# Kernel tuning notes

Hardware: AMD Instinct MI355X
Metric: run time of the kernel (lower is better)

Reference implementation:

```python
import jax, jax.numpy as jnp
import numpy as np

B, N, E = 4, 10000, 160000
D, H, HID, DE = 128, 4, 128, 16
DK = HID // H


def setup_inputs() -> dict:
    key = jax.random.key(0)
    ks = jax.random.split(key, 16)
    w = lambda k, shape: jax.random.normal(k, shape, jnp.float32) * 0.02
    return {
        "x": jax.random.normal(ks[0], (B, N, D), jnp.float32),
        "edge_index": jax.random.randint(ks[1], (2, E), 0, N, dtype=jnp.int32),
        "edge_attr": jax.random.normal(ks[2], (E, DE), jnp.float32),
        "Wq": w(ks[3], (D, HID)), "bq": jnp.zeros((HID,), jnp.float32),
        "Wk": w(ks[4], (D, HID)), "bk": jnp.zeros((HID,), jnp.float32),
        "Wv": w(ks[5], (D, HID)), "bv": jnp.zeros((HID,), jnp.float32),
        "Wf": w(ks[6], (DE, 2 * HID)), "bf": jnp.zeros((2 * HID,), jnp.float32),
        "Wo": w(ks[7], (HID, D)), "bo": jnp.zeros((D,), jnp.float32),
        "ln_g": jnp.ones((D,), jnp.float32), "ln_b": jnp.zeros((D,), jnp.float32),
    }


def reference(x, edge_index, edge_attr, Wq, bq, Wk, bk, Wv, bv, Wf, bf, Wo, bo, ln_g, ln_b):
    src, dst = edge_index[0], edge_index[1]
    # node projections -> [B, N, H, DK]
    Q = (x @ Wq + bq).reshape(B, N, H, DK)
    K = (x @ Wk + bk).reshape(B, N, H, DK)
    V = (x @ Wv + bv).reshape(B, N, H, DK)
    # edge gathers -> [B, E, H, DK]
    q_e, k_e, v_e = Q[:, dst], K[:, src], V[:, src]
    # FiLM modulation of keys (edge-conditioned, shared across batch)
    gamma, beta = jnp.split(edge_attr @ Wf + bf, 2, axis=-1)
    gamma = gamma.reshape(1, E, H, DK)
    beta = beta.reshape(1, E, H, DK)
    k_e = k_e * (1.0 + gamma) + beta
    logits = (q_e * k_e).sum(-1) / np.sqrt(DK).astype(np.float32)  # [B, E, H]

    def seg_softmax(lg):  # lg: [E, H], softmax over edges sharing a dst node
        m = jax.ops.segment_max(lg, dst, num_segments=N)       # [N, H]
        ex = jnp.exp(lg - m[dst])
        s = jax.ops.segment_sum(ex, dst, num_segments=N)        # [N, H]
        return ex / s[dst]

    att = jax.vmap(seg_softmax)(logits)                         # [B, E, H]
    msg = att[..., None] * v_e                                  # [B, E, H, DK]
    agg = jax.vmap(lambda m: jax.ops.segment_sum(m, dst, num_segments=N))(msg)
    y = agg.reshape(B, N, HID) @ Wo + bo                        # [B, N, D]
    h = x + y  # dropout is identity in eval mode
    mu = h.mean(-1, keepdims=True)
    var = ((h - mu) ** 2).mean(-1, keepdims=True)
    return (h - mu) / jnp.sqrt(var + 1e-5) * ln_g + ln_b
```

## Files before the change

kernel.cpp:

```cpp
#include <hip/hip_runtime.h>
#include <hip/hip_bf16.h>

#define B_ 4
#define N_ 10000
#define E_ 160000
#define D_ 128
#define H_ 4
#define HID_ 128
#define DK_ 32
#define DE_ 16
#define PGRID 2048
#define QKV_BLKS 625
#define FILM_BLKS 1024
#define HIST_BLKS 625

typedef __attribute__((ext_vector_type(8))) short short8v;
typedef __attribute__((ext_vector_type(4))) short short4v;
typedef __attribute__((ext_vector_type(4))) float f32x4;
typedef __attribute__((ext_vector_type(2))) float f32x2;

__device__ __forceinline__ short bfb(float f) {
  union { float f; unsigned u; } c; c.f = f;
  unsigned u = c.u + 0x7FFFu + ((c.u >> 16) & 1u);
  return (short)(u >> 16);
}
__device__ __forceinline__ float b2f(unsigned short u) {
  union { unsigned u; float f; } c; c.u = ((unsigned)u) << 16;
  return c.f;
}
__device__ __forceinline__ f32x2 fp8lo(unsigned u) {
  return __builtin_amdgcn_cvt_pk_f32_fp8((int)u, false);
}
__device__ __forceinline__ f32x2 fp8hi(unsigned u) {
  return __builtin_amdgcn_cvt_pk_f32_fp8((int)u, true);
}
__device__ __forceinline__ int pk4fp8(float a, float b, float c, float d) {
  int r = __builtin_amdgcn_cvt_pk_fp8_f32(a, b, 0, false);
  r = __builtin_amdgcn_cvt_pk_fp8_f32(c, d, r, true);
  return r;
}

__global__ __launch_bounds__(256) void wt_prep(
    const float* __restrict__ Wq, const float* __restrict__ Wk,
    const float* __restrict__ Wv, const float* __restrict__ Wo,
    const float* __restrict__ Wf,
    short* __restrict__ wt, short* __restrict__ wfb) {
  const int blk = blockIdx.x;
  if (blk < 256) {
    const float* Ws[4] = {Wq, Wk, Wv, Wo};
    const int i = blk * 256 + threadIdx.x;
    const int m = i >> 14;
    const int k = (i >> 7) & 127;
    const int n = i & 127;
    wt[(size_t)m * 16384 + n * 128 + k] = bfb(Ws[m][k * 128 + n]);
  } else {
    const int i = (blk - 256) * 256 + threadIdx.x;
    const int col = i >> 5;
    const int k = i & 31;
    wfb[col * 32 + k] = (k < DE_) ? bfb(Wf[k * 256 + col]) : (short)0;
  }
}

__global__ __launch_bounds__(256) void phase1(
    const float* __restrict__ x, const short* __restrict__ wt,
    const float* __restrict__ bq, const float* __restrict__ bk,
    const float* __restrict__ bv,
    unsigned short* __restrict__ Qb, unsigned char* __restrict__ kv8,
    const float* __restrict__ ea, const short* __restrict__ wfb,
    const float* __restrict__ bf, unsigned char* __restrict__ film8,
    const int* __restrict__ ei, int* __restrict__ cnt) {
  const int blk = blockIdx.x;

  if (blk < QKV_BLKS) {
    __shared__ short xs[4][16][136];
    const int wave = threadIdx.x >> 6;
    const int lane = threadIdx.x & 63;
    const int ln15 = lane & 15;
    const int g    = lane >> 4;
    const long rowBase = ((long)blk * 4 + wave) * 16;

    for (int i = lane; i < 16 * 32; i += 64) {
      const int r  = i >> 5;
      const int c4 = (i & 31) * 4;
      const float4 v = *(const float4*)(x + (rowBase + r) * 128 + c4);
      short4v sv; sv.x = bfb(v.x); sv.y = bfb(v.y); sv.z = bfb(v.z); sv.w = bfb(v.w);
      *(short4v*)&xs[wave][r][c4] = sv;
    }
    __syncthreads();

    short8v af[4];
#pragma unroll
    for (int kk = 0; kk < 4; ++kk)
      af[kk] = *(const short8v*)&xs[wave][ln15][kk * 32 + g * 8];

    const float* bs[3] = {bq, bk, bv};

    int bbv4[4], nnv[4];
#pragma unroll
    for (int r = 0; r < 4; ++r) {
      const long row = rowBase + g * 4 + r;
      bbv4[r] = (int)(row / N_);
      nnv[r] = (int)(row - (long)bbv4[r] * N_);
    }

#pragma unroll
    for (int m = 0; m < 3; ++m) {
      const short* Wt = wt + (size_t)m * 16384;
      f32x4 acc[8];
#pragma unroll
      for (int cb = 0; cb < 8; ++cb) acc[cb] = (f32x4){0.f, 0.f, 0.f, 0.f};

#pragma unroll
      for (int kk = 0; kk < 4; ++kk) {
#pragma unroll
        for (int cb = 0; cb < 8; ++cb) {
          const short8v bfr =
              *(const short8v*)(Wt + (ln15 * 8 + cb) * 128 + kk * 32 + g * 8);
          acc[cb] = __builtin_amdgcn_mfma_f32_16x16x32_bf16(af[kk], bfr, acc[cb], 0, 0, 0);
        }
      }

      const float* bias = bs[m];
      float bvv[8];
#pragma unroll
      for (int cb = 0; cb < 8; ++cb) bvv[cb] = bias[ln15 * 8 + cb];

#pragma unroll
      for (int r = 0; r < 4; ++r) {
        if (m == 0) {
          const long row = rowBase + g * 4 + r;
          short8v qs;
#pragma unroll
          for (int cb = 0; cb < 8; ++cb) qs[cb] = bfb(acc[cb][r] + bvv[cb]);
          *(short8v*)(Qb + row * 128 + ln15 * 8) = qs;
        } else {
          const int d0 = pk4fp8(acc[0][r] + bvv[0], acc[1][r] + bvv[1],
                                acc[2][r] + bvv[2], acc[3][r] + bvv[3]);
          const int d1 = pk4fp8(acc[4][r] + bvv[4], acc[5][r] + bvv[5],
                                acc[6][r] + bvv[6], acc[7][r] + bvv[7]);
          uint2 st; st.x = (unsigned)d0; st.y = (unsigned)d1;
          *(uint2*)(kv8 + (((size_t)nnv[r] * 4 + bbv4[r]) << 8) + (m - 1) * 128 +
                    ln15 * 8) = st;
        }
      }
    }
  } else if (blk < QKV_BLKS + FILM_BLKS) {
    const int fb_  = blk - QKV_BLKS;
    const int wave = threadIdx.x >> 6;
    const int lane = threadIdx.x & 63;
    const int ln15 = lane & 15;
    const int g    = lane >> 4;

    short8v wf[16];
#pragma unroll
    for (int cb = 0; cb < 16; ++cb)
      wf[cb] = *(const short8v*)(wfb + (ln15 * 16 + cb) * 32 + g * 8);
    float fbias[16];
#pragma unroll
    for (int cb = 0; cb < 16; ++cb) fbias[cb] = bf[ln15 * 16 + cb];

    for (int tile = fb_ * 4 + wave; tile < E_ / 16; tile += FILM_BLKS * 4) {
      const int e0 = tile * 16;
      short8v af = {0, 0, 0, 0, 0, 0, 0, 0};
      if (g < 2) {
        const float* ap = ea + (size_t)(e0 + ln15) * 16 + g * 8;
        const float4 a0 = *(const float4*)ap;
        const float4 a1 = *(const float4*)(ap + 4);
        af[0] = bfb(a0.x); af[1] = bfb(a0.y); af[2] = bfb(a0.z); af[3] = bfb(a0.w);
        af[4] = bfb(a1.x); af[5] = bfb(a1.y); af[6] = bfb(a1.z); af[7] = bfb(a1.w);
      }

#pragma unroll
      for (int half = 0; half < 2; ++half) {
        f32x4 acc[8];
#pragma unroll
        for (int c8 = 0; c8 < 8; ++c8) {
          acc[c8] = (f32x4){0.f, 0.f, 0.f, 0.f};
          acc[c8] = __builtin_amdgcn_mfma_f32_16x16x32_bf16(af, wf[half * 8 + c8],
                                                            acc[c8], 0, 0, 0);
        }
#pragma unroll
        for (int r = 0; r < 4; ++r) {
          const int d0 = pk4fp8(acc[0][r] + fbias[half * 8 + 0],
                                acc[1][r] + fbias[half * 8 + 1],
                                acc[2][r] + fbias[half * 8 + 2],
                                acc[3][r] + fbias[half * 8 + 3]);
          const int d1 = pk4fp8(acc[4][r] + fbias[half * 8 + 4],
                                acc[5][r] + fbias[half * 8 + 5],
                                acc[6][r] + fbias[half * 8 + 6],
                                acc[7][r] + fbias[half * 8 + 7]);
          uint2 st; st.x = (unsigned)d0; st.y = (unsigned)d1;
          *(uint2*)(film8 + (size_t)(e0 + 4 * g + r) * 256 + ln15 * 16 + half * 8) = st;
        }
      }
    }
  } else {
    const int e = (blk - QKV_BLKS - FILM_BLKS) * 256 + threadIdx.x;
    if (e < E_) atomicAdd(&cnt[ei[E_ + e]], 1);
  }
}

__global__ __launch_bounds__(1024) void csr_scan(const int* __restrict__ cnt,
                                                 int* __restrict__ rowptr,
                                                 int* __restrict__ fill) {
  __shared__ int part[1024];
  const int t = threadIdx.x;
  int local[10];
  int sum = 0;
#pragma unroll
  for (int i = 0; i < 10; ++i) {
    const int idx = t * 10 + i;
    local[i] = sum;
    sum += (idx < N_) ? cnt[idx] : 0;
  }
  part[t] = sum;
  __syncthreads();
  for (int off = 1; off < 1024; off <<= 1) {
    const int v = (t >= off) ? part[t - off] : 0;
    __syncthreads();
    part[t] += v;
    __syncthreads();
  }
  const int excl = (t == 0) ? 0 : part[t - 1];
#pragma unroll
  for (int i = 0; i < 10; ++i) {
    const int idx = t * 10 + i;
    if (idx <= N_) {
      const int o = excl + local[i];
      rowptr[idx] = o;
      if (idx < N_) fill[idx] = o;
    }
  }
}

__global__ __launch_bounds__(256) void csr_scatter(
    const int* __restrict__ ei, int* __restrict__ fill,
    int* __restrict__ esrc, int* __restrict__ eord) {
  const int e = blockIdx.x * 256 + threadIdx.x;
  if (e < E_) {
    const int dst = ei[E_ + e];
    const int pos = atomicAdd(&fill[dst], 1);
    esrc[pos] = ei[e];
    eord[pos] = e;
  }
}

__global__ __launch_bounds__(256) void fused_attn(
    const int* __restrict__ rowptr, const int* __restrict__ esrc,
    const int* __restrict__ eord, const unsigned char* __restrict__ film8,
    const unsigned short* __restrict__ Qb,
    const unsigned char* __restrict__ kv8, float* __restrict__ agg) {
  const int wave = threadIdx.x >> 6;
  const int lane = threadIdx.x & 63;
  const int e2 = lane >> 5;
  const int dh = (lane >> 4) & 1;
  const int b  = (lane >> 2) & 3;
  const int h  = lane & 3;
  const int col0 = h * 32 + dh * 16;

  for (int node = blockIdx.x * 4 + wave; node < N_; node += PGRID * 4) {
    const int beg = rowptr[node], end = rowptr[node + 1];

    float q[16];
    {
      const unsigned short* qp = Qb + ((size_t)b * N_ + node) * 128 + col0;
      const short8v t0 = *(const short8v*)qp;
      const short8v t1 = *(const short8v*)(qp + 8);
#pragma unroll
      for (int j = 0; j < 8; ++j) {
        q[j]     = b2f((unsigned short)t0[j]);
        q[8 + j] = b2f((unsigned short)t1[j]);
      }
    }
    float acc[16];
#pragma unroll
    for (int d = 0; d < 16; ++d) acc[d] = 0.f;
    float se = 0.f;

    for (int i0 = beg; i0 < end; i0 += 2) {
      const int ii = i0 + e2;
      const bool valid = ii < end;
      const int ic = valid ? ii : i0;
      const int src = esrc[ic];
      const int de  = eord[ic];
      const unsigned char* kp = kv8 + ((((size_t)src << 2) + b) << 8) + col0;
      const unsigned char* fp = film8 + (size_t)de * 256 + col0;
      const uint4 kw = *(const uint4*)kp;
      const uint4 vw = *(const uint4*)(kp + 128);
      const uint4 gw = *(const uint4*)fp;
      const uint4 tw = *(const uint4*)(fp + 128);
      const unsigned ks[4] = {kw.x, kw.y, kw.z, kw.w};
      const unsigned vs[4] = {vw.x, vw.y, vw.z, vw.w};
      const unsigned gs[4] = {gw.x, gw.y, gw.z, gw.w};
      const unsigned ts[4] = {tw.x, tw.y, tw.z, tw.w};

      float pacc[4] = {0.f, 0.f, 0.f, 0.f};
#pragma unroll
      for (int w = 0; w < 4; ++w) {
        const f32x2 k0 = fp8lo(ks[w]), k1 = fp8hi(ks[w]);
        const f32x2 g0 = fp8lo(gs[w]), g1 = fp8hi(gs[w]);
        const f32x2 t0 = fp8lo(ts[w]), t1 = fp8hi(ts[w]);
        float km;
        km = k0.x + fmaf(k0.x, g0.x, t0.x); pacc[w] = fmaf(q[4*w+0], km, pacc[w]);
        km = k0.y + fmaf(k0.y, g0.y, t0.y); pacc[w] = fmaf(q[4*w+1], km, pacc[w]);
        km = k1.x + fmaf(k1.x, g1.x, t1.x); pacc[w] = fmaf(q[4*w+2], km, pacc[w]);
        km = k1.y + fmaf(k1.y, g1.y, t1.y); pacc[w] = fmaf(q[4*w+3], km, pacc[w]);
      }
      float pl = (pacc[0] + pacc[1]) + (pacc[2] + pacc[3]);
      pl += __shfl_xor(pl, 16);

      float ex = __expf(pl * 0.17677669529663687f);
      ex = valid ? ex : 0.f;
      se += ex;
#pragma unroll
      for (int w = 0; w < 4; ++w) {
        const f32x2 v0 = fp8lo(vs[w]), v1 = fp8hi(vs[w]);
        acc[4*w+0] = fmaf(ex, v0.x, acc[4*w+0]);
        acc[4*w+1] = fmaf(ex, v0.y, acc[4*w+1]);
        acc[4*w+2] = fmaf(ex, v1.x, acc[4*w+2]);
        acc[4*w+3] = fmaf(ex, v1.y, acc[4*w+3]);
      }
    }

#pragma unroll
    for (int d = 0; d < 16; ++d) acc[d] += __shfl_xor(acc[d], 32);
    se += __shfl_xor(se, 32);

    if (e2 == 0) {
      const float inv = (end > beg) ? 1.f / se : 0.f;
      float* ap = agg + ((size_t)b * N_ + node) * 128 + col0;
#pragma unroll
      for (int c = 0; c < 4; ++c) {
        float4 o;
        o.x = acc[c*4+0] * inv; o.y = acc[c*4+1] * inv;
        o.z = acc[c*4+2] * inv; o.w = acc[c*4+3] * inv;
        *(float4*)(ap + c * 4) = o;
      }
    }
  }
}

__global__ __launch_bounds__(64) void out_ln_mfma(
    const float* __restrict__ agg, const short* __restrict__ wto,
    const float* __restrict__ bo, const float* __restrict__ x,
    const float* __restrict__ lng, const float* __restrict__ lnb,
    float* __restrict__ out) {
  __shared__ short as_[16][136];
  const int lane = threadIdx.x;
  const int ln15 = lane & 15;
  const int g    = lane >> 4;
  const long rowBase = (long)blockIdx.x * 16;

  for (int i = lane; i < 16 * 32; i += 64) {
    const int r  = i >> 5;
    const int c4 = (i & 31) * 4;
    const float4 v = *(const float4*)(agg + (rowBase + r) * 128 + c4);
    short4v sv; sv.x = bfb(v.x); sv.y = bfb(v.y); sv.z = bfb(v.z); sv.w = bfb(v.w);
    *(short4v*)&as_[r][c4] = sv;
  }
  __syncthreads();

  short8v af[4];
#pragma unroll
  for (int kk = 0; kk < 4; ++kk)
    af[kk] = *(const short8v*)&as_[ln15][kk * 32 + g * 8];

  f32x4 acc[8];
#pragma unroll
  for (int cb = 0; cb < 8; ++cb) acc[cb] = (f32x4){0.f, 0.f, 0.f, 0.f};

#pragma unroll
  for (int kk = 0; kk < 4; ++kk) {
#pragma unroll
    for (int cb = 0; cb < 8; ++cb) {
      const short8v bfr =
          *(const short8v*)(wto + (cb * 16 + ln15) * 128 + kk * 32 + g * 8);
      acc[cb] = __builtin_amdgcn_mfma_f32_16x16x32_bf16(af[kk], bfr, acc[cb], 0, 0, 0);
    }
  }

#pragma unroll
  for (int cb = 0; cb < 8; ++cb) {
    const int col = cb * 16 + ln15;
    const float bov = bo[col];
#pragma unroll
    for (int r = 0; r < 4; ++r) {
      const long row = rowBase + g * 4 + r;
      acc[cb][r] += bov + x[row * 128 + col];
    }
  }

  float s1[4], s2[4];
#pragma unroll
  for (int r = 0; r < 4; ++r) {
    s1[r] = 0.f; s2[r] = 0.f;
#pragma unroll
    for (int cb = 0; cb < 8; ++cb) {
      s1[r] += acc[cb][r];
      s2[r] = fmaf(acc[cb][r], acc[cb][r], s2[r]);
    }
  }
#pragma unroll
  for (int m = 1; m < 16; m <<= 1) {
#pragma unroll
    for (int r = 0; r < 4; ++r) {
      s1[r] += __shfl_xor(s1[r], m);
      s2[r] += __shfl_xor(s2[r], m);
    }
  }
  float mu[4], inv[4];
#pragma unroll
  for (int r = 0; r < 4; ++r) {
    mu[r] = s1[r] * (1.f / 128.f);
    const float var = s2[r] * (1.f / 128.f) - mu[r] * mu[r];
    inv[r] = rsqrtf(var + 1e-5f);
  }

#pragma unroll
  for (int cb = 0; cb < 8; ++cb) {
    const int col = cb * 16 + ln15;
    const float gv = lng[col], bv_ = lnb[col];
#pragma unroll
    for (int r = 0; r < 4; ++r) {
      const long row = rowBase + g * 4 + r;
      out[row * 128 + col] = (acc[cb][r] - mu[r]) * inv[r] * gv + bv_;
    }
  }
}

extern "C" void kernel_launch(void* const* d_in, const int* in_sizes, int n_in,
                              void* d_out, int out_size, void* d_ws, size_t ws_size,
                              hipStream_t stream) {
  const float* x   = (const float*)d_in[0];
  const int*   ei  = (const int*)d_in[1];
  const float* ea  = (const float*)d_in[2];
  const float* Wq  = (const float*)d_in[3];
  const float* bq  = (const float*)d_in[4];
  const float* Wk  = (const float*)d_in[5];
  const float* bk  = (const float*)d_in[6];
  const float* Wv  = (const float*)d_in[7];
  const float* bv  = (const float*)d_in[8];
  const float* Wf  = (const float*)d_in[9];
  const float* bf  = (const float*)d_in[10];
  const float* Wo  = (const float*)d_in[11];
  const float* bo  = (const float*)d_in[12];
  const float* lng = (const float*)d_in[13];
  const float* lnb = (const float*)d_in[14];
  float* out = (float*)d_out;

  const size_t NQ = (size_t)B_ * N_ * HID_;

  char* base = (char*)d_ws;
  size_t off = 0;
  unsigned short* Qb = (unsigned short*)(base + off); off += NQ * 2;
  float* agg  = (float*)(base + off); off += NQ * 4;
  unsigned char* kv8 = (unsigned char*)(base + off);
  off += (size_t)B_ * N_ * 256;
  unsigned char* film8 = (unsigned char*)(base + off);
  off += (size_t)E_ * 256;
  short* wt   = (short*)(base + off); off += 4 * 16384 * 2;
  short* wfb  = (short*)(base + off); off += 256 * 32 * 2;
  int*  cnt    = (int*)(base + off); off += N_ * 4;
  int*  rowptr = (int*)(base + off); off += (N_ + 1) * 4;
  int*  fill   = (int*)(base + off); off += N_ * 4;
  int*  esrc   = (int*)(base + off); off += E_ * 4;
  int*  eord   = (int*)(base + off); off += E_ * 4;

  hipMemsetAsync(cnt, 0, N_ * sizeof(int), stream);

  wt_prep<<<288, 256, 0, stream>>>(Wq, Wk, Wv, Wo, Wf, wt, wfb);
  phase1<<<QKV_BLKS + FILM_BLKS + HIST_BLKS, 256, 0, stream>>>(
      x, wt, bq, bk, bv, Qb, kv8, ea, wfb, bf, film8, ei, cnt);
  csr_scan<<<1, 1024, 0, stream>>>(cnt, rowptr, fill);
  csr_scatter<<<(E_ + 255) / 256, 256, 0, stream>>>(ei, fill, esrc, eord);
  fused_attn<<<PGRID, 256, 0, stream>>>(rowptr, esrc, eord, film8, Qb, kv8, agg);
  out_ln_mfma<<<(B_ * N_) / 16, 64, 0, stream>>>(agg, wt + 3 * 16384, bo, x, lng, lnb, out);
}
```

Before: 159.1 us.

## Fuse attention aggregation with output projection and LayerNorm; fold memset into prep

Merges the attention kernel and the output-projection/LayerNorm kernel. Each wave processes 4 nodes across all 4 batches and stages the normalized aggregates as bf16 in shared memory, then runs the MFMA projection, residual and LayerNorm directly. This removes the fp32 agg round-trip through global memory and one kernel launch. The cnt memset is also moved into extra blocks of the weight-prep kernel. The grid drops to 625 blocks with a fixed 4 nodes per wave, which may reduce parallelism and load balance across the degree-skewed nodes.

```diff
diff --git a/kernel.cpp b/kernel.cpp
--- a/kernel.cpp
+++ b/kernel.cpp
@@ -9,7 +9,6 @@
 #define HID_ 128
 #define DK_ 32
 #define DE_ 16
-#define PGRID 2048
 #define QKV_BLKS 625
 #define FILM_BLKS 1024
 #define HIST_BLKS 625
@@ -44,7 +43,7 @@
     const float* __restrict__ Wq, const float* __restrict__ Wk,
     const float* __restrict__ Wv, const float* __restrict__ Wo,
     const float* __restrict__ Wf,
-    short* __restrict__ wt, short* __restrict__ wfb) {
+    short* __restrict__ wt, short* __restrict__ wfb, int* __restrict__ cnt) {
   const int blk = blockIdx.x;
   if (blk < 256) {
     const float* Ws[4] = {Wq, Wk, Wv, Wo};
@@ -53,11 +52,14 @@
     const int k = (i >> 7) & 127;
     const int n = i & 127;
     wt[(size_t)m * 16384 + n * 128 + k] = bfb(Ws[m][k * 128 + n]);
-  } else {
+  } else if (blk < 288) {
     const int i = (blk - 256) * 256 + threadIdx.x;
     const int col = i >> 5;
     const int k = i & 31;
     wfb[col * 32 + k] = (k < DE_) ? bfb(Wf[k * 256 + col]) : (short)0;
+  } else {
+    const int i = (blk - 288) * 256 + threadIdx.x;
+    if (i < N_) cnt[i] = 0;
   }
 }
 
@@ -245,11 +247,14 @@
   }
 }
 
-__global__ __launch_bounds__(256) void fused_attn(
+__global__ __launch_bounds__(256) void attn_ln(
     const int* __restrict__ rowptr, const int* __restrict__ esrc,
     const int* __restrict__ eord, const unsigned char* __restrict__ film8,
-    const unsigned short* __restrict__ Qb,
-    const unsigned char* __restrict__ kv8, float* __restrict__ agg) {
+    const unsigned short* __restrict__ Qb, const unsigned char* __restrict__ kv8,
+    const float* __restrict__ x, const short* __restrict__ wto,
+    const float* __restrict__ bo, const float* __restrict__ lng,
+    const float* __restrict__ lnb, float* __restrict__ out) {
+  __shared__ short as_[4][16][136];
   const int wave = threadIdx.x >> 6;
   const int lane = threadIdx.x & 63;
   const int e2 = lane >> 5;
@@ -257,8 +262,10 @@
   const int b  = (lane >> 2) & 3;
   const int h  = lane & 3;
   const int col0 = h * 32 + dh * 16;
-
-  for (int node = blockIdx.x * 4 + wave; node < N_; node += PGRID * 4) {
+  const int grp = blockIdx.x * 4 + wave;
+
+  for (int nn = 0; nn < 4; ++nn) {
+    const int node = grp * 4 + nn;
     const int beg = rowptr[node], end = rowptr[node + 1];
 
     float q[16];
@@ -328,46 +335,29 @@
 
     if (e2 == 0) {
       const float inv = (end > beg) ? 1.f / se : 0.f;
-      float* ap = agg + ((size_t)b * N_ + node) * 128 + col0;
-#pragma unroll
-      for (int c = 0; c < 4; ++c) {
-        float4 o;
-        o.x = acc[c*4+0] * inv; o.y = acc[c*4+1] * inv;
-        o.z = acc[c*4+2] * inv; o.w = acc[c*4+3] * inv;
-        *(float4*)(ap + c * 4) = o;
-      }
-    }
-  }
-}
-
-__global__ __launch_bounds__(64) void out_ln_mfma(
-    const float* __restrict__ agg, const short* __restrict__ wto,
-    const float* __restrict__ bo, const float* __restrict__ x,
-    const float* __restrict__ lng, const float* __restrict__ lnb,
-    float* __restrict__ out) {
-  __shared__ short as_[16][136];
-  const int lane = threadIdx.x;
+#pragma unroll
+      for (int c4 = 0; c4 < 4; ++c4) {
+        short4v sv;
+#pragma unroll
+        for (int j = 0; j < 4; ++j) sv[j] = bfb(acc[c4 * 4 + j] * inv);
+        *(short4v*)&as_[wave][nn * 4 + b][col0 + c4 * 4] = sv;
+      }
+    }
+  }
+
+  __syncthreads();
+
   const int ln15 = lane & 15;
   const int g    = lane >> 4;
-  const long rowBase = (long)blockIdx.x * 16;
-
-  for (int i = lane; i < 16 * 32; i += 64) {
-    const int r  = i >> 5;
-    const int c4 = (i & 31) * 4;
-    const float4 v = *(const float4*)(agg + (rowBase + r) * 128 + c4);
-    short4v sv; sv.x = bfb(v.x); sv.y = bfb(v.y); sv.z = bfb(v.z); sv.w = bfb(v.w);
-    *(short4v*)&as_[r][c4] = sv;
-  }
-  __syncthreads();
 
   short8v af[4];
 #pragma unroll
   for (int kk = 0; kk < 4; ++kk)
-    af[kk] = *(const short8v*)&as_[ln15][kk * 32 + g * 8];
-
-  f32x4 acc[8];
-#pragma unroll
-  for (int cb = 0; cb < 8; ++cb) acc[cb] = (f32x4){0.f, 0.f, 0.f, 0.f};
+    af[kk] = *(const short8v*)&as_[wave][ln15][kk * 32 + g * 8];
+
+  f32x4 acc2[8];
+#pragma unroll
+  for (int cb = 0; cb < 8; ++cb) acc2[cb] = (f32x4){0.f, 0.f, 0.f, 0.f};
 
 #pragma unroll
   for (int kk = 0; kk < 4; ++kk) {
@@ -375,19 +365,21 @@
     for (int cb = 0; cb < 8; ++cb) {
       const short8v bfr =
           *(const short8v*)(wto + (cb * 16 + ln15) * 128 + kk * 32 + g * 8);
-      acc[cb] = __builtin_amdgcn_mfma_f32_16x16x32_bf16(af[kk], bfr, acc[cb], 0, 0, 0);
-    }
-  }
+      acc2[cb] = __builtin_amdgcn_mfma_f32_16x16x32_bf16(af[kk], bfr, acc2[cb], 0, 0, 0);
+    }
+  }
+
+  long grow[4];
+#pragma unroll
+  for (int r = 0; r < 4; ++r) grow[r] = (long)r * N_ + grp * 4 + g;
 
 #pragma unroll
   for (int cb = 0; cb < 8; ++cb) {
     const int col = cb * 16 + ln15;
     const float bov = bo[col];
 #pragma unroll
-    for (int r = 0; r < 4; ++r) {
-      const long row = rowBase + g * 4 + r;
-      acc[cb][r] += bov + x[row * 128 + col];
-    }
+    for (int r = 0; r < 4; ++r)
+      acc2[cb][r] += bov + x[grow[r] * 128 + col];
   }
 
   float s1[4], s2[4];
@@ -396,8 +388,8 @@
     s1[r] = 0.f; s2[r] = 0.f;
 #pragma unroll
     for (int cb = 0; cb < 8; ++cb) {
-      s1[r] += acc[cb][r];
-      s2[r] = fmaf(acc[cb][r], acc[cb][r], s2[r]);
+      s1[r] += acc2[cb][r];
+      s2[r] = fmaf(acc2[cb][r], acc2[cb][r], s2[r]);
     }
   }
 #pragma unroll
@@ -408,12 +400,12 @@
       s2[r] += __shfl_xor(s2[r], m);
     }
   }
-  float mu[4], inv[4];
+  float mu[4], inv2[4];
 #pragma unroll
   for (int r = 0; r < 4; ++r) {
     mu[r] = s1[r] * (1.f / 128.f);
     const float var = s2[r] * (1.f / 128.f) - mu[r] * mu[r];
-    inv[r] = rsqrtf(var + 1e-5f);
+    inv2[r] = rsqrtf(var + 1e-5f);
   }
 
 #pragma unroll
@@ -421,10 +413,8 @@
     const int col = cb * 16 + ln15;
     const float gv = lng[col], bv_ = lnb[col];
 #pragma unroll
-    for (int r = 0; r < 4; ++r) {
-      const long row = rowBase + g * 4 + r;
-      out[row * 128 + col] = (acc[cb][r] - mu[r]) * inv[r] * gv + bv_;
-    }
+    for (int r = 0; r < 4; ++r)
+      out[grow[r] * 128 + col] = (acc2[cb][r] - mu[r]) * inv2[r] * gv + bv_;
   }
 }
 
@@ -453,7 +443,6 @@
   char* base = (char*)d_ws;
   size_t off = 0;
   unsigned short* Qb = (unsigned short*)(base + off); off += NQ * 2;
-  float* agg  = (float*)(base + off); off += NQ * 4;
   unsigned char* kv8 = (unsigned char*)(base + off);
   off += (size_t)B_ * N_ * 256;
   unsigned char* film8 = (unsigned char*)(base + off);
@@ -466,13 +455,11 @@
   int*  esrc   = (int*)(base + off); off += E_ * 4;
   int*  eord   = (int*)(base + off); off += E_ * 4;
 
-  hipMemsetAsync(cnt, 0, N_ * sizeof(int), stream);
-
-  wt_prep<<<288, 256, 0, stream>>>(Wq, Wk, Wv, Wo, Wf, wt, wfb);
+  wt_prep<<<328, 256, 0, stream>>>(Wq, Wk, Wv, Wo, Wf, wt, wfb, cnt);
   phase1<<<QKV_BLKS + FILM_BLKS + HIST_BLKS, 256, 0, stream>>>(
       x, wt, bq, bk, bv, Qb, kv8, ea, wfb, bf, film8, ei, cnt);
   csr_scan<<<1, 1024, 0, stream>>>(cnt, rowptr, fill);
   csr_scatter<<<(E_ + 255) / 256, 256, 0, stream>>>(ei, fill, esrc, eord);
-  fused_attn<<<PGRID, 256, 0, stream>>>(rowptr, esrc, eord, film8, Qb, kv8, agg);
-  out_ln_mfma<<<(B_ * N_) / 16, 64, 0, stream>>>(agg, wt + 3 * 16384, bo, x, lng, lnb, out);
-}
+  attn_ln<<<625, 256, 0, stream>>>(rowptr, esrc, eord, film8, Qb, kv8,
+                                   x, wt + 3 * 16384, bo, lng, lnb, out);
+}
```

Result: no change. 159.7 us (+0.4%).
